# Kernel optimization log

Hardware: AMD Instinct MI355X
Metric: run time of the kernel (lower is better)

Reference implementation:

```python
import jax, jax.numpy as jnp
import numpy as np


def setup_inputs() -> dict:
    key = jax.random.key(0)
    k1, k2, *kw = jax.random.split(key, 12)
    N, E = 10000, 320000
    D_IN, D_HID, D_EMB, D_PRED = 2, 128, 256, 128

    def lin(k, fan_in, fan_out):
        bound = 1.0 / np.sqrt(fan_in)
        kw_, kb_ = jax.random.split(k)
        W = jax.random.uniform(kw_, (fan_in, fan_out), jnp.float32, -bound, bound)
        b = jax.random.uniform(kb_, (fan_out,), jnp.float32, -bound, bound)
        return W, b

    W1, b1 = lin(kw[0], D_IN, D_HID)
    W2, b2 = lin(kw[1], D_HID, D_EMB)
    Wp1, bp1 = lin(kw[2], D_EMB, D_PRED)
    Wp2, bp2 = lin(kw[3], D_PRED, 1)

    src = jax.random.randint(k1, (E,), 0, N, dtype=jnp.int32)
    dst = jax.random.randint(k2, (E,), 0, N, dtype=jnp.int32)
    return {
        "W1": W1, "b1": b1, "W2": W2, "b2": b2,
        "Wp1": Wp1, "bp1": bp1, "Wp2": Wp2, "bp2": bp2,
        "src": src, "dst": dst, "num_nodes": N,
    }


def reference(W1, b1, W2, b2, Wp1, bp1, Wp2, bp2, src, dst, num_nodes):
    N = num_nodes
    E = src.shape[0]
    ones = jnp.ones((E,), jnp.float32)
    # node features = [in_degree, out_degree]  -> [N, 2]
    in_deg = jax.ops.segment_sum(ones, dst, num_segments=N)
    out_deg = jax.ops.segment_sum(ones, src, num_segments=N)
    x = jnp.stack([in_deg, out_deg], axis=1)

    def gcn_agg(h):
        # sum of messages from source nodes into destination nodes (SpMM-like)
        return jax.ops.segment_sum(h[src], dst, num_segments=N)

    h = jax.nn.relu(gcn_agg(x) @ W1 + b1)        # [N, 128]
    h = gcn_agg(h) @ W2 + b2                     # [N, 256]
    h = jax.nn.relu(h)
    graph_embedding = jnp.sum(h, axis=0)         # [256] (dgl.sum_nodes, single graph)
    m = jax.nn.relu(graph_embedding @ Wp1 + bp1)
    metric = m @ Wp2 + bp2                       # [1]
    return (graph_embedding, metric)
```

## Files before the change

kernel.cpp:

```cpp
#include <hip/hip_runtime.h>

#define N_NODES 10000
#define CAPLOG 7
#define CAP 128
#define NPART 16
#define NBH 128
#define TBH 512

__global__ __launch_bounds__(TBH) void hist_kernel(const int* __restrict__ src,
                                                   const int* __restrict__ dst,
                                                   unsigned int* __restrict__ cnt, int E) {
  __shared__ unsigned int hist[N_NODES];
  const int tid = threadIdx.x, bid = blockIdx.x;
  for (int i = tid; i < N_NODES; i += TBH) hist[i] = 0;
  __syncthreads();
  const int chunk = (E + NBH - 1) / NBH;
  const int e0 = bid * chunk, e1 = min(E, e0 + chunk);
  for (int e = e0 + tid; e < e1; e += TBH) {
    atomicAdd(&hist[dst[e]], 1u);
    atomicAdd(&hist[src[e]], 0x10000u);
  }
  __syncthreads();
  unsigned int* outb = cnt + (size_t)bid * N_NODES;
  for (int i = tid; i < N_NODES; i += TBH) outb[i] = hist[i];
}

__global__ __launch_bounds__(256) void scan_kernel(const unsigned int* __restrict__ cnt,
                                                   unsigned int* __restrict__ off,
                                                   unsigned int* __restrict__ pack) {
  const int n = blockIdx.x * 256 + threadIdx.x;
  if (n >= N_NODES) return;
  unsigned run_in = 0, run_out = 0;
  for (int b = 0; b < NBH; ++b) {
    unsigned v = cnt[(size_t)b * N_NODES + n];
    off[(size_t)b * N_NODES + n] = run_in;
    run_in += v & 0xFFFFu;
    run_out += v >> 16;
  }
  pack[n] = run_in | (run_out << 16);
}

__global__ __launch_bounds__(TBH) void scatter_kernel(const int* __restrict__ src,
                                                      const int* __restrict__ dst,
                                                      const unsigned int* __restrict__ off,
                                                      unsigned short* __restrict__ slots,
                                                      int E) {
  __shared__ unsigned int cur[N_NODES];
  const int tid = threadIdx.x, bid = blockIdx.x;
  const unsigned int* ob = off + (size_t)bid * N_NODES;
  for (int i = tid; i < N_NODES; i += TBH) cur[i] = ob[i];
  __syncthreads();
  const int chunk = (E + NBH - 1) / NBH;
  const int e0 = bid * chunk, e1 = min(E, e0 + chunk);
  for (int e = e0 + tid; e < e1; e += TBH) {
    int d = dst[e];
    unsigned idx = atomicAdd(&cur[d], 1u);
    if (idx < CAP) slots[(d << CAPLOG) + idx] = (unsigned short)src[e];
  }
}

__global__ __launch_bounds__(256) void agg1_kernel(const unsigned int* __restrict__ pack,
                                                   const unsigned short* __restrict__ slots,
                                                   float2* __restrict__ a) {
  const int tid = threadIdx.x;
  const int hw = tid >> 5, hl = tid & 31;
  const int node = blockIdx.x * 8 + hw;
  const int deg = min((int)(pack[node] & 0xFFFFu), CAP);
  const int base = node << CAPLOG;
  float a0 = 0.f, a1 = 0.f;
  for (int e = hl; e < deg; e += 32) {
    unsigned v = pack[slots[base + e]];
    a0 += (float)(v & 0xFFFFu);
    a1 += (float)(v >> 16);
  }
#pragma unroll
  for (int off = 16; off > 0; off >>= 1) {
    a0 += __shfl_xor(a0, off);
    a1 += __shfl_xor(a1, off);
  }
  if (hl == 0) a[node] = make_float2(a0, a1);
}

__global__ __launch_bounds__(256) void agg2gemm2_kernel(const unsigned int* __restrict__ pack,
                                                        const unsigned short* __restrict__ slots,
                                                        const float2* __restrict__ a,
                                                        const float* __restrict__ W1,
                                                        const float* __restrict__ b1,
                                                        const float* __restrict__ W2,
                                                        const float* __restrict__ b2,
                                                        float* __restrict__ ge_p) {
  __shared__ float s_tile[8][128];
  const int tid = threadIdx.x, bid = blockIdx.x;
  const int hw = tid >> 5, hl = tid & 31;

  float w10[4], w11[4], bb[4];
#pragma unroll
  for (int c = 0; c < 4; ++c) {
    w10[c] = W1[4 * hl + c];
    w11[c] = W1[128 + 4 * hl + c];
    bb[c] = b1[4 * hl + c];
  }
  const int node = bid * 8 + hw;
  const int deg = min((int)(pack[node] & 0xFFFFu), CAP);
  float acc0 = 0.f, acc1 = 0.f, acc2 = 0.f, acc3 = 0.f;
  int rem = deg, eb = node << CAPLOG;
  while (rem > 0) {
    int cnt = min(rem, 32);
    float va0 = 0.f, va1 = 0.f;
    if (hl < cnt) {
      float2 av = a[slots[eb + hl]];
      va0 = av.x;
      va1 = av.y;
    }
    for (int j = 0; j < cnt; ++j) {
      float x0 = __shfl(va0, j, 32);
      float x1 = __shfl(va1, j, 32);
      acc0 += fmaxf(fmaf(x0, w10[0], fmaf(x1, w11[0], bb[0])), 0.f);
      acc1 += fmaxf(fmaf(x0, w10[1], fmaf(x1, w11[1], bb[1])), 0.f);
      acc2 += fmaxf(fmaf(x0, w10[2], fmaf(x1, w11[2], bb[2])), 0.f);
      acc3 += fmaxf(fmaf(x0, w10[3], fmaf(x1, w11[3], bb[3])), 0.f);
    }
    rem -= cnt;
    eb += cnt;
  }
  s_tile[hw][4 * hl + 0] = acc0;
  s_tile[hw][4 * hl + 1] = acc1;
  s_tile[hw][4 * hl + 2] = acc2;
  s_tile[hw][4 * hl + 3] = acc3;
  __syncthreads();

  float d[8];
#pragma unroll
  for (int n = 0; n < 8; ++n) d[n] = 0.f;
#pragma unroll
  for (int kc = 0; kc < 4; ++kc) {
    float wv[32];
#pragma unroll
    for (int c = 0; c < 32; ++c) wv[c] = W2[(kc * 32 + c) * 256 + tid];
#pragma unroll
    for (int n = 0; n < 8; ++n) {
      const float4* row4 = (const float4*)&s_tile[n][kc * 32];
      float t0 = 0.f, t1 = 0.f, t2 = 0.f, t3 = 0.f;
#pragma unroll
      for (int q = 0; q < 8; ++q) {
        float4 rv = row4[q];
        t0 = fmaf(rv.x, wv[4 * q + 0], t0);
        t1 = fmaf(rv.y, wv[4 * q + 1], t1);
        t2 = fmaf(rv.z, wv[4 * q + 2], t2);
        t3 = fmaf(rv.w, wv[4 * q + 3], t3);
      }
      d[n] += (t0 + t1) + (t2 + t3);
    }
  }

  const float bj = b2[tid];
  float accge = 0.f;
#pragma unroll
  for (int n = 0; n < 8; ++n) accge += fmaxf(d[n] + bj, 0.f);
  atomicAdd(&ge_p[((bid & (NPART - 1)) << 8) + tid], accge);
}

__global__ __launch_bounds__(256) void head_kernel(const float* __restrict__ ge_p,
                                                   const float* __restrict__ Wp1,
                                                   const float* __restrict__ bp1,
                                                   const float* __restrict__ Wp2,
                                                   const float* __restrict__ bp2,
                                                   float* __restrict__ out) {
  __shared__ float s_ge[256];
  __shared__ float s_m[256];
  int tid = threadIdx.x;
  float g = 0.f;
#pragma unroll
  for (int p = 0; p < NPART; ++p) g += ge_p[p * 256 + tid];
  s_ge[tid] = g;
  out[tid] = g;
  __syncthreads();
  int j = tid & 127, halfk = tid >> 7;
  float d = halfk ? 0.f : bp1[j];
  int k0 = halfk << 7;
#pragma unroll 8
  for (int k = k0; k < k0 + 128; ++k) d = fmaf(s_ge[k], Wp1[k * 128 + j], d);
  s_m[tid] = d;
  __syncthreads();
  if (tid < 128) s_m[tid] = fmaxf(s_m[tid] + s_m[tid + 128], 0.f) * Wp2[tid];
  __syncthreads();
  if (tid < 64) {
    float v = s_m[tid] + s_m[tid + 64];
#pragma unroll
    for (int off = 32; off > 0; off >>= 1) v += __shfl_xor(v, off);
    if (tid == 0) out[256] = v + bp2[0];
  }
}

extern "C" void kernel_launch(void* const* d_in, const int* in_sizes, int n_in,
                              void* d_out, int out_size, void* d_ws, size_t ws_size,
                              hipStream_t stream) {
  const float* W1 = (const float*)d_in[0];
  const float* b1 = (const float*)d_in[1];
  const float* W2 = (const float*)d_in[2];
  const float* b2 = (const float*)d_in[3];
  const float* Wp1 = (const float*)d_in[4];
  const float* bp1 = (const float*)d_in[5];
  const float* Wp2 = (const float*)d_in[6];
  const float* bp2 = (const float*)d_in[7];
  const int* src = (const int*)d_in[8];
  const int* dst = (const int*)d_in[9];
  const int E = in_sizes[8];
  const int N = N_NODES;

  char* p = (char*)d_ws;
  float* ge_p = (float*)p;               p += (size_t)NPART * 256 * 4;
  unsigned int* pack = (unsigned int*)p; p += (size_t)N * 4;
  unsigned short* slots = (unsigned short*)p; p += (size_t)N * CAP * 2;
  float2* a = (float2*)p;                p += (size_t)N * 8;
  unsigned int* cnt = (unsigned int*)p;  p += (size_t)NBH * N * 4;
  unsigned int* off = (unsigned int*)p;
  float* out = (float*)d_out;

  hipMemsetAsync(d_ws, 0, (size_t)NPART * 256 * 4, stream);

  hist_kernel<<<NBH, TBH, 0, stream>>>(src, dst, cnt, E);
  scan_kernel<<<(N + 255) / 256, 256, 0, stream>>>(cnt, off, pack);
  scatter_kernel<<<NBH, TBH, 0, stream>>>(src, dst, off, slots, E);
  agg1_kernel<<<N / 8, 256, 0, stream>>>(pack, slots, a);
  agg2gemm2_kernel<<<N / 8, 256, 0, stream>>>(pack, slots, a, W1, b1, W2, b2, ge_p);
  head_kernel<<<1, 256, 0, stream>>>(ge_p, Wp1, bp1, Wp2, bp2, out);
}
```

Measured before the change: 132.4 us.

## Split degree scan into segments, fold memset, retile agg2/GEMM2 for 16 nodes

The serial 128-step per-node scan over block histograms is split into 8 parallel segments plus a second pass, which exposes more parallelism across the grid. The separate memset is folded into the histogram kernel. The agg2+GEMM2 kernel now handles 16 nodes per block with a 4x4 register tile and float4 W2 loads, halving the block count and W2 re-reads. The first GEMM loop is a leftover dead computation whose results are zeroed before the real loop, which wastes work unless the compiler removes it. The packed in/out counts are summed jointly in segments, which risks 16-bit overflow in the low half, and the zeroing of ge_p in block 0 is not ordered against other blocks.

```diff
diff --git a/kernel.cpp b/kernel.cpp
--- a/kernel.cpp
+++ b/kernel.cpp
@@ -6,12 +6,17 @@
 #define NPART 16
 #define NBH 128
 #define TBH 512
+#define NSEG 8
+#define SEGW 16
 
 __global__ __launch_bounds__(TBH) void hist_kernel(const int* __restrict__ src,
                                                    const int* __restrict__ dst,
-                                                   unsigned int* __restrict__ cnt, int E) {
+                                                   unsigned int* __restrict__ cnt,
+                                                   float* __restrict__ ge_p, int E) {
   __shared__ unsigned int hist[N_NODES];
   const int tid = threadIdx.x, bid = blockIdx.x;
+  if (bid == 0)
+    for (int i = tid; i < NPART * 256; i += TBH) ge_p[i] = 0.f;
   for (int i = tid; i < N_NODES; i += TBH) hist[i] = 0;
   __syncthreads();
   const int chunk = (E + NBH - 1) / NBH;
@@ -25,30 +30,48 @@
   for (int i = tid; i < N_NODES; i += TBH) outb[i] = hist[i];
 }
 
-__global__ __launch_bounds__(256) void scan_kernel(const unsigned int* __restrict__ cnt,
-                                                   unsigned int* __restrict__ off,
-                                                   unsigned int* __restrict__ pack) {
+__global__ __launch_bounds__(256) void scan1_kernel(const unsigned int* __restrict__ cnt,
+                                                    unsigned int* __restrict__ off,
+                                                    unsigned int* __restrict__ psum) {
+  const int n = blockIdx.x * 256 + threadIdx.x;
+  const int seg = blockIdx.y;
+  if (n >= N_NODES) return;
+  unsigned run = 0;
+  for (int i = 0; i < SEGW; ++i) {
+    const size_t idx = (size_t)(seg * SEGW + i) * N_NODES + n;
+    unsigned v = cnt[idx];
+    off[idx] = run;
+    run += v;
+  }
+  psum[(size_t)seg * N_NODES + n] = run;
+}
+
+__global__ __launch_bounds__(256) void scan2_kernel(const unsigned int* __restrict__ psum,
+                                                    unsigned int* __restrict__ sbase,
+                                                    unsigned int* __restrict__ pack) {
   const int n = blockIdx.x * 256 + threadIdx.x;
   if (n >= N_NODES) return;
-  unsigned run_in = 0, run_out = 0;
-  for (int b = 0; b < NBH; ++b) {
-    unsigned v = cnt[(size_t)b * N_NODES + n];
-    off[(size_t)b * N_NODES + n] = run_in;
-    run_in += v & 0xFFFFu;
-    run_out += v >> 16;
-  }
-  pack[n] = run_in | (run_out << 16);
+  unsigned base = 0;
+#pragma unroll
+  for (int seg = 0; seg < NSEG; ++seg) {
+    sbase[(size_t)seg * N_NODES + n] = base;
+    base += psum[(size_t)seg * N_NODES + n];
+  }
+  pack[n] = base;
 }
 
 __global__ __launch_bounds__(TBH) void scatter_kernel(const int* __restrict__ src,
                                                       const int* __restrict__ dst,
                                                       const unsigned int* __restrict__ off,
+                                                      const unsigned int* __restrict__ sbase,
                                                       unsigned short* __restrict__ slots,
                                                       int E) {
   __shared__ unsigned int cur[N_NODES];
   const int tid = threadIdx.x, bid = blockIdx.x;
   const unsigned int* ob = off + (size_t)bid * N_NODES;
-  for (int i = tid; i < N_NODES; i += TBH) cur[i] = ob[i];
+  const unsigned int* sb = sbase + (size_t)(bid / SEGW) * N_NODES;
+  for (int i = tid; i < N_NODES; i += TBH)
+    cur[i] = (ob[i] & 0xFFFFu) + (sb[i] & 0xFFFFu);
   __syncthreads();
   const int chunk = (E + NBH - 1) / NBH;
   const int e0 = bid * chunk, e1 = min(E, e0 + chunk);
@@ -74,9 +97,9 @@
     a1 += (float)(v >> 16);
   }
 #pragma unroll
-  for (int off = 16; off > 0; off >>= 1) {
-    a0 += __shfl_xor(a0, off);
-    a1 += __shfl_xor(a1, off);
+  for (int o = 16; o > 0; o >>= 1) {
+    a0 += __shfl_xor(a0, o);
+    a1 += __shfl_xor(a1, o);
   }
   if (hl == 0) a[node] = make_float2(a0, a1);
 }
@@ -89,7 +112,7 @@
                                                         const float* __restrict__ W2,
                                                         const float* __restrict__ b2,
                                                         float* __restrict__ ge_p) {
-  __shared__ float s_tile[8][128];
+  __shared__ float s_tile[16][128];
   const int tid = threadIdx.x, bid = blockIdx.x;
   const int hw = tid >> 5, hl = tid & 31;
 
@@ -100,64 +123,102 @@
     w11[c] = W1[128 + 4 * hl + c];
     bb[c] = b1[4 * hl + c];
   }
-  const int node = bid * 8 + hw;
-  const int deg = min((int)(pack[node] & 0xFFFFu), CAP);
-  float acc0 = 0.f, acc1 = 0.f, acc2 = 0.f, acc3 = 0.f;
-  int rem = deg, eb = node << CAPLOG;
-  while (rem > 0) {
-    int cnt = min(rem, 32);
-    float va0 = 0.f, va1 = 0.f;
-    if (hl < cnt) {
-      float2 av = a[slots[eb + hl]];
-      va0 = av.x;
-      va1 = av.y;
+#pragma unroll
+  for (int jn = 0; jn < 2; ++jn) {
+    const int node = bid * 16 + hw * 2 + jn;
+    const int deg = min((int)(pack[node] & 0xFFFFu), CAP);
+    float acc0 = 0.f, acc1 = 0.f, acc2 = 0.f, acc3 = 0.f;
+    int rem = deg, eb = node << CAPLOG;
+    while (rem > 0) {
+      int cnt = min(rem, 32);
+      float va0 = 0.f, va1 = 0.f;
+      if (hl < cnt) {
+        float2 av = a[slots[eb + hl]];
+        va0 = av.x;
+        va1 = av.y;
+      }
+      for (int jj = 0; jj < cnt; ++jj) {
+        float x0 = __shfl(va0, jj, 32);
+        float x1 = __shfl(va1, jj, 32);
+        acc0 += fmaxf(fmaf(x0, w10[0], fmaf(x1, w11[0], bb[0])), 0.f);
+        acc1 += fmaxf(fmaf(x0, w10[1], fmaf(x1, w11[1], bb[1])), 0.f);
+        acc2 += fmaxf(fmaf(x0, w10[2], fmaf(x1, w11[2], bb[2])), 0.f);
+        acc3 += fmaxf(fmaf(x0, w10[3], fmaf(x1, w11[3], bb[3])), 0.f);
+      }
+      rem -= cnt;
+      eb += cnt;
     }
-    for (int j = 0; j < cnt; ++j) {
-      float x0 = __shfl(va0, j, 32);
-      float x1 = __shfl(va1, j, 32);
-      acc0 += fmaxf(fmaf(x0, w10[0], fmaf(x1, w11[0], bb[0])), 0.f);
-      acc1 += fmaxf(fmaf(x0, w10[1], fmaf(x1, w11[1], bb[1])), 0.f);
-      acc2 += fmaxf(fmaf(x0, w10[2], fmaf(x1, w11[2], bb[2])), 0.f);
-      acc3 += fmaxf(fmaf(x0, w10[3], fmaf(x1, w11[3], bb[3])), 0.f);
+    s_tile[hw * 2 + jn][4 * hl + 0] = acc0;
+    s_tile[hw * 2 + jn][4 * hl + 1] = acc1;
+    s_tile[hw * 2 + jn][4 * hl + 2] = acc2;
+    s_tile[hw * 2 + jn][4 * hl + 3] = acc3;
+  }
+  __syncthreads();
+
+  const int qt = tid >> 6;
+  const int c4 = (tid & 63) * 4;
+  float d[4][4];
+#pragma unroll
+  for (int r = 0; r < 4; ++r)
+#pragma unroll
+    for (int c = 0; c < 4; ++c) d[r][c] = 0.f;
+#pragma unroll
+  for (int kc = 0; kc < 8; ++kc) {
+    float4 wv[16];
+#pragma unroll
+    for (int c = 0; c < 16; ++c)
+      wv[c] = *(const float4*)&W2[(kc * 16 + c) * 256 + c4];
+#pragma unroll
+    for (int r = 0; r < 4; ++r) {
+      const float4* row4 = (const float4*)&s_tile[4 * qt + r][kc * 16];
+#pragma unroll
+      for (int q = 0; q < 4; ++q) {
+        float4 rv = row4[q];
+#pragma unroll
+        for (int c = 0; c < 4; ++c) {
+          d[r][c] = fmaf(rv.x, wv[4 * q + 0].x * 0.f + (&wv[4 * q + 0].x)[c], d[r][c]);
+        }
+      }
     }
-    rem -= cnt;
-    eb += cnt;
-  }
-  s_tile[hw][4 * hl + 0] = acc0;
-  s_tile[hw][4 * hl + 1] = acc1;
-  s_tile[hw][4 * hl + 2] = acc2;
-  s_tile[hw][4 * hl + 3] = acc3;
-  __syncthreads();
-
-  float d[8];
-#pragma unroll
-  for (int n = 0; n < 8; ++n) d[n] = 0.f;
-#pragma unroll
-  for (int kc = 0; kc < 4; ++kc) {
-    float wv[32];
-#pragma unroll
-    for (int c = 0; c < 32; ++c) wv[c] = W2[(kc * 32 + c) * 256 + tid];
-#pragma unroll
-    for (int n = 0; n < 8; ++n) {
-      const float4* row4 = (const float4*)&s_tile[n][kc * 32];
-      float t0 = 0.f, t1 = 0.f, t2 = 0.f, t3 = 0.f;
-#pragma unroll
-      for (int q = 0; q < 8; ++q) {
+  }
+#pragma unroll
+  for (int r = 0; r < 4; ++r)
+#pragma unroll
+    for (int c = 0; c < 4; ++c) d[r][c] = 0.f;
+#pragma unroll
+  for (int kc = 0; kc < 8; ++kc) {
+    float4 wv[16];
+#pragma unroll
+    for (int c = 0; c < 16; ++c)
+      wv[c] = *(const float4*)&W2[(kc * 16 + c) * 256 + c4];
+#pragma unroll
+    for (int r = 0; r < 4; ++r) {
+      const float4* row4 = (const float4*)&s_tile[4 * qt + r][kc * 16];
+#pragma unroll
+      for (int q = 0; q < 4; ++q) {
         float4 rv = row4[q];
-        t0 = fmaf(rv.x, wv[4 * q + 0], t0);
-        t1 = fmaf(rv.y, wv[4 * q + 1], t1);
-        t2 = fmaf(rv.z, wv[4 * q + 2], t2);
-        t3 = fmaf(rv.w, wv[4 * q + 3], t3);
-      }
-      d[n] += (t0 + t1) + (t2 + t3);
+        float4 w0 = wv[4 * q + 0], w1 = wv[4 * q + 1], w2v = wv[4 * q + 2], w3 = wv[4 * q + 3];
+        d[r][0] = fmaf(rv.x, w0.x, d[r][0]); d[r][1] = fmaf(rv.x, w0.y, d[r][1]);
+        d[r][2] = fmaf(rv.x, w0.z, d[r][2]); d[r][3] = fmaf(rv.x, w0.w, d[r][3]);
+        d[r][0] = fmaf(rv.y, w1.x, d[r][0]); d[r][1] = fmaf(rv.y, w1.y, d[r][1]);
+        d[r][2] = fmaf(rv.y, w1.z, d[r][2]); d[r][3] = fmaf(rv.y, w1.w, d[r][3]);
+        d[r][0] = fmaf(rv.z, w2v.x, d[r][0]); d[r][1] = fmaf(rv.z, w2v.y, d[r][1]);
+        d[r][2] = fmaf(rv.z, w2v.z, d[r][2]); d[r][3] = fmaf(rv.z, w2v.w, d[r][3]);
+        d[r][0] = fmaf(rv.w, w3.x, d[r][0]); d[r][1] = fmaf(rv.w, w3.y, d[r][1]);
+        d[r][2] = fmaf(rv.w, w3.z, d[r][2]); d[r][3] = fmaf(rv.w, w3.w, d[r][3]);
+      }
     }
   }
 
-  const float bj = b2[tid];
-  float accge = 0.f;
-#pragma unroll
-  for (int n = 0; n < 8; ++n) accge += fmaxf(d[n] + bj, 0.f);
-  atomicAdd(&ge_p[((bid & (NPART - 1)) << 8) + tid], accge);
+  const int part = (bid & (NPART - 1)) << 8;
+#pragma unroll
+  for (int c = 0; c < 4; ++c) {
+    const float bj = b2[c4 + c];
+    float g = 0.f;
+#pragma unroll
+    for (int r = 0; r < 4; ++r) g += fmaxf(d[r][c] + bj, 0.f);
+    atomicAdd(&ge_p[part + c4 + c], g);
+  }
 }
 
 __global__ __launch_bounds__(256) void head_kernel(const float* __restrict__ ge_p,
@@ -214,15 +275,16 @@
   unsigned short* slots = (unsigned short*)p; p += (size_t)N * CAP * 2;
   float2* a = (float2*)p;                p += (size_t)N * 8;
   unsigned int* cnt = (unsigned int*)p;  p += (size_t)NBH * N * 4;
-  unsigned int* off = (unsigned int*)p;
+  unsigned int* off = (unsigned int*)p;  p += (size_t)NBH * N * 4;
+  unsigned int* psum = (unsigned int*)p; p += (size_t)NSEG * N * 4;
+  unsigned int* sbase = (unsigned int*)p;
   float* out = (float*)d_out;
 
-  hipMemsetAsync(d_ws, 0, (size_t)NPART * 256 * 4, stream);
-
-  hist_kernel<<<NBH, TBH, 0, stream>>>(src, dst, cnt, E);
-  scan_kernel<<<(N + 255) / 256, 256, 0, stream>>>(cnt, off, pack);
-  scatter_kernel<<<NBH, TBH, 0, stream>>>(src, dst, off, slots, E);
+  hist_kernel<<<NBH, TBH, 0, stream>>>(src, dst, cnt, ge_p, E);
+  scan1_kernel<<<dim3((N + 255) / 256, NSEG), 256, 0, stream>>>(cnt, off, psum);
+  scan2_kernel<<<(N + 255) / 256, 256, 0, stream>>>(psum, sbase, pack);
+  scatter_kernel<<<NBH, TBH, 0, stream>>>(src, dst, off, sbase, slots, E);
   agg1_kernel<<<N / 8, 256, 0, stream>>>(pack, slots, a);
-  agg2gemm2_kernel<<<N / 8, 256, 0, stream>>>(pack, slots, a, W1, b1, W2, b2, ge_p);
+  agg2gemm2_kernel<<<N / 16, 256, 0, stream>>>(pack, slots, a, W1, b1, W2, b2, ge_p);
   head_kernel<<<1, 256, 0, stream>>>(ge_p, Wp1, bp1, Wp2, bp2, out);
 }
```

Result: slower. 142.3 us (+7.5%).
